# Kernel tuning notes

Hardware: AMD Instinct MI355X
Metric: run time of the kernel (lower is better)

Reference implementation:

```python
import jax, jax.numpy as jnp
import numpy as np
from jax import lax

B, L, D, H = 32, 512, 1024, 1024


def setup_inputs() -> dict:
    key = jax.random.key(0)
    kx, kw, kb = jax.random.split(key, 3)
    x = jax.random.normal(kx, (B, L, D), dtype=jnp.float32)
    # nn.Linear(D+H, 4H): weight (4H, D+H), bias (4H,), uniform(-1/sqrt(fan_in), 1/sqrt(fan_in))
    bound = 1.0 / np.sqrt(D + H)
    W = jax.random.uniform(kw, (4 * H, D + H), minval=-bound, maxval=bound, dtype=jnp.float32)
    b = jax.random.uniform(kb, (4 * H,), minval=-bound, maxval=bound, dtype=jnp.float32)
    return {"x": x, "W": W, "b": b}


def reference(x, W, b):
    Bsz, Lseq, Din = x.shape
    Hd = W.shape[0] // 4

    def step(carry, x_t):
        h, c = carry
        combined = jnp.concatenate([h, x_t], axis=-1)          # (B, H+D)
        gates = combined @ W.T + b                              # (B, 4H)
        f, i, o, c_tilde = jnp.split(gates, 4, axis=-1)
        c_new = jax.nn.sigmoid(f) * c + jax.nn.sigmoid(i) * jnp.tanh(c_tilde)
        h_new = jax.nn.sigmoid(o) * jnp.tanh(c_new)
        return (h_new, c_new), h_new

    h0 = jnp.zeros((Bsz, Hd), dtype=x.dtype)
    c0 = jnp.zeros((Bsz, Hd), dtype=x.dtype)
    xs = jnp.transpose(x, (1, 0, 2))                            # (L, B, D)
    _, hs = lax.scan(step, (h0, c0), xs)                        # hs: (L, B, H)
    return jnp.transpose(hs, (1, 0, 2))                         # (B, L, H)
```

## Files before the change

kernel.cpp:

```cpp
#include <hip/hip_runtime.h>
#include <hip/hip_fp16.h>

#define B_SZ 32
#define L_SZ 512
#define D_SZ 1024
#define H_SZ 1024
#define NG   4096
#define M_SZ 16384

typedef __attribute__((ext_vector_type(8))) short short8;
typedef __attribute__((ext_vector_type(4))) float f32x4;
typedef __attribute__((ext_vector_type(4))) unsigned u32x4;
typedef __attribute__((ext_vector_type(4))) unsigned short u16x4;

static const size_t GX_OFF  = 0;
static const size_t XB_OFF  = 134217728;
static const size_t WH_OFF  = 167772160;
static const size_t WX_OFF  = 176160768;
static const size_t FLG_OFF = 184680448;

__device__ __forceinline__ unsigned short f2bf(float f) {
  union { float f; unsigned u; } v; v.f = f;
  unsigned r = v.u + 0x7fffu + ((v.u >> 16) & 1u);
  return (unsigned short)(r >> 16);
}

__device__ __forceinline__ void gload_lds16(const void* g, void* l) {
  __builtin_amdgcn_global_load_lds(
      (const __attribute__((address_space(1))) unsigned*)g,
      (__attribute__((address_space(3))) unsigned*)l, 16, 0, 0);
}


__global__ __launch_bounds__(256) void k_convert_w(const float* __restrict__ W,
                                                   unsigned short* __restrict__ Wh,
                                                   unsigned short* __restrict__ Wx) {
  int idx = blockIdx.x * 256 + threadIdx.x;
  f32x4 v = ((const f32x4*)W)[idx];
  u16x4 o;
#pragma unroll
  for (int e = 0; e < 4; ++e) o[e] = f2bf(v[e]);
  int n   = idx >> 9;
  int col = (idx & 511) * 4;
  if (col < 1024) *(u16x4*)(Wh + (size_t)n * 1024 + col)          = o;
  else            *(u16x4*)(Wx + (size_t)n * 1024 + (col - 1024)) = o;
}

__global__ __launch_bounds__(256) void k_convert_x(const float* __restrict__ x,
                                                   unsigned short* __restrict__ xb) {
  int idx = blockIdx.x * 256 + threadIdx.x;
  f32x4 v = ((const f32x4*)x)[idx];
  u16x4 o;
#pragma unroll
  for (int e = 0; e < 4; ++e) o[e] = f2bf(v[e]);
  unsigned long long val;
  __builtin_memcpy(&val, &o, 8);
  unsigned short* p = xb + (size_t)idx * 4;
  asm volatile("global_store_dwordx2 %0, %1, off sc0 sc1"
               :: "v"(p), "v"(val) : "memory");
}

__global__ __launch_bounds__(256) void k_zero_wt(unsigned* __restrict__ p, int n) {
  int i = blockIdx.x * 256 + threadIdx.x;
  unsigned z = 0u;
  if (i < n)
    asm volatile("global_store_dword %0, %1, off sc0 sc1"
                 :: "v"(p + i), "v"(z) : "memory");
}


__global__ __launch_bounds__(256) void k_xgemm(const unsigned short* __restrict__ A,
                                               const unsigned short* __restrict__ Bw,
                                               __half* __restrict__ C) {
  __shared__ unsigned short sA[128 * 64];
  __shared__ unsigned short sB[128 * 64];
  const int m0 = blockIdx.x * 128;
  const int n0 = blockIdx.y * 128;
  const int tid = threadIdx.x;
  const int lane = tid & 63;
  const int w = tid >> 6;
  const int wm = w >> 1, wn = w & 1;
  f32x4 acc[4][4] = {};
  for (int k0 = 0; k0 < 1024; k0 += 64) {
#pragma unroll
    for (int it = 0; it < 4; ++it) {
      int chunk = it * 256 + w * 64 + lane;
      int row = chunk >> 3, kc = chunk & 7;
      gload_lds16(A + (size_t)(m0 + row) * 1024 + k0 + kc * 8,
                  (char*)sA + (size_t)(it * 256 + w * 64) * 16);
      gload_lds16(Bw + (size_t)(n0 + row) * 1024 + k0 + kc * 8,
                  (char*)sB + (size_t)(it * 256 + w * 64) * 16);
    }
    asm volatile("s_waitcnt vmcnt(0)" ::: "memory");
    __syncthreads();
#pragma unroll
    for (int ks = 0; ks < 2; ++ks) {
      short8 af[4], bfr[4];
#pragma unroll
      for (int i = 0; i < 4; ++i) {
        int arow = wm * 64 + i * 16 + (lane & 15);
        af[i] = *(const short8*)(sA + arow * 64 + ks * 32 + (lane >> 4) * 8);
      }
#pragma unroll
      for (int j = 0; j < 4; ++j) {
        int brow = wn * 64 + j * 16 + (lane & 15);
        bfr[j] = *(const short8*)(sB + brow * 64 + ks * 32 + (lane >> 4) * 8);
      }
#pragma unroll
      for (int i = 0; i < 4; ++i)
#pragma unroll
        for (int j = 0; j < 4; ++j)
          acc[i][j] = __builtin_amdgcn_mfma_f32_16x16x32_bf16(af[i], bfr[j], acc[i][j], 0, 0, 0);
    }
    __syncthreads();
  }
#pragma unroll
  for (int i = 0; i < 4; ++i)
#pragma unroll
    for (int j = 0; j < 4; ++j)
#pragma unroll
      for (int q = 0; q < 4; ++q) {
        int row = m0 + wm * 64 + i * 16 + (lane >> 4) * 4 + q;
        int col = n0 + wn * 64 + j * 16 + (lane & 15);
        C[(size_t)row * NG + col] = __float2half(acc[i][j][q]);
      }
}


__global__ __launch_bounds__(256) void k_lstm(const unsigned short* __restrict__ Whg,
                                              const __half* __restrict__ Gx,
                                              const float* __restrict__ bias,
                                              unsigned short* __restrict__ ring,
                                              float* __restrict__ out,
                                              unsigned* __restrict__ flags) {
  extern __shared__ char lds[];
  char* w_base = lds;
  char* h_base = lds + 65536;
  float* gates_s = (float*)(lds + 131072);
  float* bias_s  = (float*)(lds + 131072 + 4224);
  float* c_s     = (float*)(lds + 131072 + 4224 + 128);
  unsigned short* hlds = (unsigned short*)(lds + 131072 + 4224 + 128 + 1024);

  const int tid = threadIdx.x;
  const int lane = tid & 63;
  const int w = tid >> 6;
  const int wg = blockIdx.x;
  const int j0 = wg * 8;

  __builtin_amdgcn_fence(__ATOMIC_ACQUIRE, "agent");

  for (int i = tid; i < 4096; i += 256) {
    int c = i >> 7, kc = i & 127;
    int n = (c >> 3) * 1024 + j0 + (c & 7);
    u32x4 v = *(const u32x4*)(Whg + (size_t)n * 1024 + kc * 8);
    *(u32x4*)(w_base + c * 2048 + ((kc * 16) ^ ((c & 7) << 4))) = v;
  }
  if (tid < 32) bias_s[tid] = bias[(tid >> 3) * 1024 + j0 + (tid & 7)];
  c_s[tid] = 0.f;
  __syncthreads();

  const int mt = w >> 1, nt = w & 1;
  const int arow = mt * 16 + (lane & 15);
  const int brow = nt * 16 + (lane & 15);
  const char* aBase = h_base + arow * 2048;
  const char* bBase = w_base + brow * 2048;
  const int kslot = (lane >> 4) * 16;
  const int aswz = (arow & 7) << 4;
  const int bswz = (brow & 7) << 4;
  const int b_ = tid >> 3, jj = tid & 7;
  const float rb0 = bias_s[jj], rb1 = bias_s[8 + jj];
  const float rb2 = bias_s[16 + jj], rb3 = bias_s[24 + jj];

  const unsigned* fp0 = flags + (size_t)(2 * tid) * 16;
  const unsigned* fp1 = flags + (size_t)(2 * tid + 1) * 16;

  for (int t = 0; t < 512; ++t) {
    const unsigned short* hin = ring + (size_t)t * 32768;
    unsigned short* hout = (unsigned short*)ring + (size_t)(t + 1) * 32768;

    u32x4 hz = {0u, 0u, 0u, 0u};
    u32x4 h0=hz,h1=hz,h2=hz,h3=hz,h4=hz,h5=hz,h6=hz,h7=hz,
          h8=hz,h9=hz,h10=hz,h11=hz,h12=hz,h13=hz,h14=hz,h15=hz;
    if (t) {
#define HLD(r, it) asm volatile("global_load_dwordx4 %0, %1, off" \
      : "=v"(r) : "v"((const char*)hin + (size_t)((it) * 256 + tid) * 16) : "memory")
      HLD(h0,0); HLD(h1,1); HLD(h2,2); HLD(h3,3);
      HLD(h4,4); HLD(h5,5); HLD(h6,6); HLD(h7,7);
      HLD(h8,8); HLD(h9,9); HLD(h10,10); HLD(h11,11);
      HLD(h12,12); HLD(h13,13); HLD(h14,14); HLD(h15,15);
#undef HLD
    }
    const char* gxp = (const char*)(Gx + ((size_t)(b_ * L_SZ + t)) * NG + j0 + jj);
    unsigned gxa, gxb, gxc, gxd;
    asm volatile("global_load_ushort %0, %1, off" : "=v"(gxa) : "v"(gxp)        : "memory");
    asm volatile("global_load_ushort %0, %1, off" : "=v"(gxb) : "v"(gxp + 2048) : "memory");
    asm volatile("global_load_ushort %0, %1, off" : "=v"(gxc) : "v"(gxp + 4096) : "memory");
    asm volatile("global_load_ushort %0, %1, off" : "=v"(gxd) : "v"(gxp + 6144) : "memory");

#define HWR(r, it) { int i_ = (it) * 256 + tid; int bb_ = i_ >> 7, kc_ = i_ & 127; \
      *(u32x4*)(h_base + bb_ * 2048 + ((kc_ * 16) ^ ((bb_ & 7) << 4))) = r; }
    asm volatile("s_waitcnt vmcnt(12)" ::: "memory");
    HWR(h0,0); HWR(h1,1); HWR(h2,2); HWR(h3,3);
    HWR(h4,4); HWR(h5,5); HWR(h6,6); HWR(h7,7);
    asm volatile("s_waitcnt vmcnt(4)" ::: "memory");
    HWR(h8,8); HWR(h9,9); HWR(h10,10); HWR(h11,11);
    HWR(h12,12); HWR(h13,13); HWR(h14,14); HWR(h15,15);
#undef HWR
    __syncthreads();

    f32x4 acc = {0.f, 0.f, 0.f, 0.f};
#pragma unroll
    for (int ks = 0; ks < 32; ++ks) {
      int kb = ks * 64 + kslot;
      short8 a  = *(const short8*)(aBase + (kb ^ aswz));
      short8 bv = *(const short8*)(bBase + (kb ^ bswz));
      acc = __builtin_amdgcn_mfma_f32_16x16x32_bf16(a, bv, acc, 0, 0, 0);
    }
    __syncthreads();
#pragma unroll
    for (int q = 0; q < 4; ++q)
      gates_s[(mt * 16 + (lane >> 4) * 4 + q) * 33 + nt * 16 + (lane & 15)] = acc[q];
    __syncthreads();

    asm volatile("s_waitcnt vmcnt(0)" ::: "memory");
    float hn;
    {
      float sf = gates_s[b_ * 33 + jj]      + __half2float(__ushort_as_half((unsigned short)gxa)) + rb0;
      float si = gates_s[b_ * 33 + 8 + jj]  + __half2float(__ushort_as_half((unsigned short)gxb)) + rb1;
      float so = gates_s[b_ * 33 + 16 + jj] + __half2float(__ushort_as_half((unsigned short)gxc)) + rb2;
      float sc = gates_s[b_ * 33 + 24 + jj] + __half2float(__ushort_as_half((unsigned short)gxd)) + rb3;
      float gf = 1.f / (1.f + expf(-sf));
      float gi = 1.f / (1.f + expf(-si));
      float go = 1.f / (1.f + expf(-so));
      float cn = gf * c_s[tid] + gi * tanhf(sc);
      hn = go * tanhf(cn);
      c_s[tid] = cn;
      hlds[b_ * 8 + jj] = f2bf(hn);
    }
    float* outp = out + ((size_t)b_ * L_SZ + t) * H_SZ + j0 + jj;

    if (t < 511) {
      __syncthreads();
      if (tid < 32) {
        u32x4 v = *(u32x4*)(hlds + tid * 8);
        unsigned short* hp = hout + (size_t)tid * H_SZ + j0;
        asm volatile("global_store_dwordx4 %0, %1, off sc0 sc1"
                     :: "v"(hp), "v"(v) : "memory");
      }
      asm volatile("s_waitcnt vmcnt(0)" ::: "memory");
      if (tid == 0) {
        unsigned fv = (unsigned)(t + 1);
        const unsigned* myf = flags + (size_t)wg * 16;
        asm volatile("global_store_dword %0, %1, off sc0 sc1"
                     :: "v"(myf), "v"(fv) : "memory");
      }
      *outp = hn;
      if (tid < 64) {
        unsigned fa, fb;
        do {
          asm volatile("global_load_dword %0, %2, off sc0 sc1\n\t"
                       "global_load_dword %1, %3, off sc0 sc1\n\t"
                       "s_waitcnt vmcnt(0)"
                       : "=v"(fa), "=v"(fb) : "v"(fp0), "v"(fp1) : "memory");
        } while (!__all(fa > (unsigned)t && fb > (unsigned)t));
      }
      __syncthreads();
    } else {
      *outp = hn;
    }
  }
}


extern "C" void kernel_launch(void* const* d_in, const int* in_sizes, int n_in,
                              void* d_out, int out_size, void* d_ws, size_t ws_size,
                              hipStream_t stream) {
  const float* x = (const float*)d_in[0];
  const float* W = (const float*)d_in[1];
  const float* b = (const float*)d_in[2];
  char* ws = (char*)d_ws;
  __half* Gx           = (__half*)(ws + GX_OFF);
  unsigned short* xb   = (unsigned short*)(ws + XB_OFF);
  unsigned short* Wh   = (unsigned short*)(ws + WH_OFF);
  unsigned short* Wx   = (unsigned short*)(ws + WX_OFF);
  unsigned* flags      = (unsigned*)(ws + FLG_OFF);
  float* out = (float*)d_out;

  k_convert_w<<<8192, 256, 0, stream>>>(W, Wh, Wx);
  k_convert_x<<<16384, 256, 0, stream>>>(x, xb);
  k_zero_wt<<<8, 256, 0, stream>>>(flags, 8192 / 4);

  k_xgemm<<<dim3(128, 32), 256, 0, stream>>>(xb, Wx, Gx);

  hipFuncSetAttribute((const void*)k_lstm,
                      hipFuncAttributeMaxDynamicSharedMemorySize, 137472);
  k_lstm<<<128, 256, 137472, stream>>>(Wh, Gx, b, xb, out, flags);
}
```

Before: 2.389 ms.

## Load recurrent h MFMA fragments directly from global into registers, skip LDS staging

The recurrent step no longer stages the previous hidden state through LDS. Each lane loads its own MFMA A-operand fragments straight from the global ring buffer into registers, and staged vmcnt waits overlap those loads with MFMAs split across two accumulators. This removes the LDS write, a barrier and the LDS reads from the serial per-step critical path, and it shrinks LDS use. The cell state also moves from LDS into a register. The cost is higher VGPR pressure from 32 vector registers of h per lane, and each wave refetches h rows redundantly from global/L2.

```diff
diff --git a/kernel.cpp b/kernel.cpp
--- a/kernel.cpp
+++ b/kernel.cpp
@@ -127,19 +127,17 @@
 }
 
 
-__global__ __launch_bounds__(256) void k_lstm(const unsigned short* __restrict__ Whg,
-                                              const __half* __restrict__ Gx,
-                                              const float* __restrict__ bias,
-                                              unsigned short* __restrict__ ring,
-                                              float* __restrict__ out,
-                                              unsigned* __restrict__ flags) {
+__global__ __launch_bounds__(256, 1) void k_lstm(const unsigned short* __restrict__ Whg,
+                                                 const __half* __restrict__ Gx,
+                                                 const float* __restrict__ bias,
+                                                 unsigned short* __restrict__ ring,
+                                                 float* __restrict__ out,
+                                                 unsigned* __restrict__ flags) {
   extern __shared__ char lds[];
   char* w_base = lds;
-  char* h_base = lds + 65536;
-  float* gates_s = (float*)(lds + 131072);
-  float* bias_s  = (float*)(lds + 131072 + 4224);
-  float* c_s     = (float*)(lds + 131072 + 4224 + 128);
-  unsigned short* hlds = (unsigned short*)(lds + 131072 + 4224 + 128 + 1024);
+  float* gates_s = (float*)(lds + 65536);
+  float* bias_s  = (float*)(lds + 65536 + 4224);
+  unsigned short* hlds = (unsigned short*)(lds + 65536 + 4224 + 128);
 
   const int tid = threadIdx.x;
   const int lane = tid & 63;
@@ -156,40 +154,26 @@
     *(u32x4*)(w_base + c * 2048 + ((kc * 16) ^ ((c & 7) << 4))) = v;
   }
   if (tid < 32) bias_s[tid] = bias[(tid >> 3) * 1024 + j0 + (tid & 7)];
-  c_s[tid] = 0.f;
   __syncthreads();
 
   const int mt = w >> 1, nt = w & 1;
-  const int arow = mt * 16 + (lane & 15);
   const int brow = nt * 16 + (lane & 15);
-  const char* aBase = h_base + arow * 2048;
   const char* bBase = w_base + brow * 2048;
   const int kslot = (lane >> 4) * 16;
-  const int aswz = (arow & 7) << 4;
   const int bswz = (brow & 7) << 4;
   const int b_ = tid >> 3, jj = tid & 7;
   const float rb0 = bias_s[jj], rb1 = bias_s[8 + jj];
   const float rb2 = bias_s[16 + jj], rb3 = bias_s[24 + jj];
+  const size_t a_off = (size_t)(mt * 16 + (lane & 15)) * 2048 + (size_t)(lane >> 4) * 16;
+  float c_reg = 0.f;
 
   const unsigned* fp0 = flags + (size_t)(2 * tid) * 16;
   const unsigned* fp1 = flags + (size_t)(2 * tid + 1) * 16;
 
   for (int t = 0; t < 512; ++t) {
-    const unsigned short* hin = ring + (size_t)t * 32768;
-    unsigned short* hout = (unsigned short*)ring + (size_t)(t + 1) * 32768;
-
-    u32x4 hz = {0u, 0u, 0u, 0u};
-    u32x4 h0=hz,h1=hz,h2=hz,h3=hz,h4=hz,h5=hz,h6=hz,h7=hz,
-          h8=hz,h9=hz,h10=hz,h11=hz,h12=hz,h13=hz,h14=hz,h15=hz;
-    if (t) {
-#define HLD(r, it) asm volatile("global_load_dwordx4 %0, %1, off" \
-      : "=v"(r) : "v"((const char*)hin + (size_t)((it) * 256 + tid) * 16) : "memory")
-      HLD(h0,0); HLD(h1,1); HLD(h2,2); HLD(h3,3);
-      HLD(h4,4); HLD(h5,5); HLD(h6,6); HLD(h7,7);
-      HLD(h8,8); HLD(h9,9); HLD(h10,10); HLD(h11,11);
-      HLD(h12,12); HLD(h13,13); HLD(h14,14); HLD(h15,15);
-#undef HLD
-    }
+    const char* aG = (const char*)ring + (size_t)t * 65536 + a_off;
+    unsigned short* hout = ring + (size_t)(t + 1) * 32768;
+
     const char* gxp = (const char*)(Gx + ((size_t)(b_ * L_SZ + t)) * NG + j0 + jj);
     unsigned gxa, gxb, gxc, gxd;
     asm volatile("global_load_ushort %0, %1, off" : "=v"(gxa) : "v"(gxp)        : "memory");
@@ -197,26 +181,44 @@
     asm volatile("global_load_ushort %0, %1, off" : "=v"(gxc) : "v"(gxp + 4096) : "memory");
     asm volatile("global_load_ushort %0, %1, off" : "=v"(gxd) : "v"(gxp + 6144) : "memory");
 
-#define HWR(r, it) { int i_ = (it) * 256 + tid; int bb_ = i_ >> 7, kc_ = i_ & 127; \
-      *(u32x4*)(h_base + bb_ * 2048 + ((kc_ * 16) ^ ((bb_ & 7) << 4))) = r; }
-    asm volatile("s_waitcnt vmcnt(12)" ::: "memory");
-    HWR(h0,0); HWR(h1,1); HWR(h2,2); HWR(h3,3);
-    HWR(h4,4); HWR(h5,5); HWR(h6,6); HWR(h7,7);
-    asm volatile("s_waitcnt vmcnt(4)" ::: "memory");
-    HWR(h8,8); HWR(h9,9); HWR(h10,10); HWR(h11,11);
-    HWR(h12,12); HWR(h13,13); HWR(h14,14); HWR(h15,15);
-#undef HWR
-    __syncthreads();
-
-    f32x4 acc = {0.f, 0.f, 0.f, 0.f};
-#pragma unroll
-    for (int ks = 0; ks < 32; ++ks) {
-      int kb = ks * 64 + kslot;
-      short8 a  = *(const short8*)(aBase + (kb ^ aswz));
-      short8 bv = *(const short8*)(bBase + (kb ^ bswz));
-      acc = __builtin_amdgcn_mfma_f32_16x16x32_bf16(a, bv, acc, 0, 0, 0);
-    }
-    __syncthreads();
+    u32x4 areg[32];
+    if (t) {
+#pragma unroll
+      for (int ks = 0; ks < 32; ++ks)
+        asm volatile("global_load_dwordx4 %0, %1, off offset:%2"
+                     : "=v"(areg[ks]) : "v"(aG), "n"(ks * 64) : "memory");
+    } else {
+#pragma unroll
+      for (int ks = 0; ks < 32; ++ks) areg[ks] = (u32x4){0u, 0u, 0u, 0u};
+    }
+
+    f32x4 acc0 = {0.f, 0.f, 0.f, 0.f}, acc1 = {0.f, 0.f, 0.f, 0.f};
+#pragma unroll
+    for (int g = 0; g < 4; ++g) {
+      short8 bfr[8];
+#pragma unroll
+      for (int k = 0; k < 8; ++k) {
+        int ks = g * 8 + k;
+        bfr[k] = *(const short8*)(bBase + ((ks * 64 + kslot) ^ bswz));
+      }
+      if (t) {
+        if (g == 0)      asm volatile("s_waitcnt vmcnt(24)" ::: "memory");
+        else if (g == 1) asm volatile("s_waitcnt vmcnt(16)" ::: "memory");
+        else if (g == 2) asm volatile("s_waitcnt vmcnt(8)"  ::: "memory");
+        else             asm volatile("s_waitcnt vmcnt(0)"  ::: "memory");
+        __builtin_amdgcn_sched_barrier(0);
+      }
+#pragma unroll
+      for (int k = 0; k < 8; k += 2) {
+        int ks = g * 8 + k;
+        short8 a0, a1;
+        __builtin_memcpy(&a0, &areg[ks], 16);
+        __builtin_memcpy(&a1, &areg[ks + 1], 16);
+        acc0 = __builtin_amdgcn_mfma_f32_16x16x32_bf16(a0, bfr[k],     acc0, 0, 0, 0);
+        acc1 = __builtin_amdgcn_mfma_f32_16x16x32_bf16(a1, bfr[k + 1], acc1, 0, 0, 0);
+      }
+    }
+    f32x4 acc = acc0 + acc1;
 #pragma unroll
     for (int q = 0; q < 4; ++q)
       gates_s[(mt * 16 + (lane >> 4) * 4 + q) * 33 + nt * 16 + (lane & 15)] = acc[q];
@@ -232,10 +234,10 @@
       float gf = 1.f / (1.f + expf(-sf));
       float gi = 1.f / (1.f + expf(-si));
       float go = 1.f / (1.f + expf(-so));
-      float cn = gf * c_s[tid] + gi * tanhf(sc);
+      float cn = gf * c_reg + gi * tanhf(sc);
       hn = go * tanhf(cn);
-      c_s[tid] = cn;
-      hlds[b_ * 8 + jj] = f2bf(hn);
+      c_reg = cn;
+      hlds[tid] = f2bf(hn);
     }
     float* outp = out + ((size_t)b_ * L_SZ + t) * H_SZ + j0 + jj;
 
@@ -293,6 +295,6 @@
   k_xgemm<<<dim3(128, 32), 256, 0, stream>>>(xb, Wx, Gx);
 
   hipFuncSetAttribute((const void*)k_lstm,
-                      hipFuncAttributeMaxDynamicSharedMemorySize, 137472);
-  k_lstm<<<128, 256, 137472, stream>>>(Wh, Gx, b, xb, out, flags);
-}
+                      hipFuncAttributeMaxDynamicSharedMemorySize, 70400);
+  k_lstm<<<128, 256, 70400, stream>>>(Wh, Gx, b, xb, out, flags);
+}
```

Result: slower. 3.546 ms (+48.4%).

## Keep recurrent weight slice in registers and split K across waves

Applied to the files above, without the earlier changes.

The recurrent LSTM kernel no longer stages its slice of Wh in LDS. Each wave holds its 256-wide K slice of the weight fragments in registers and computes all 32x32 gate outputs for that K range with four MFMA accumulators. The four per-wave partial sums are reduced through LDS, and the cell state moves from LDS to a register. This cuts LDS weight reads and the per-step LDS footprint, at the cost of higher register pressure (launch_bounds 256,1) and an extra partial-sum reduction on each step.

```diff
diff --git a/kernel.cpp b/kernel.cpp
--- a/kernel.cpp
+++ b/kernel.cpp
@@ -127,63 +127,65 @@
 }
 
 
-__global__ __launch_bounds__(256) void k_lstm(const unsigned short* __restrict__ Whg,
-                                              const __half* __restrict__ Gx,
-                                              const float* __restrict__ bias,
-                                              unsigned short* __restrict__ ring,
-                                              float* __restrict__ out,
-                                              unsigned* __restrict__ flags) {
+__global__ __launch_bounds__(256, 1) void k_lstm(const unsigned short* __restrict__ Whg,
+                                                 const __half* __restrict__ Gx,
+                                                 const float* __restrict__ bias,
+                                                 unsigned short* __restrict__ ring,
+                                                 float* __restrict__ out,
+                                                 unsigned* __restrict__ flags) {
   extern __shared__ char lds[];
-  char* w_base = lds;
-  char* h_base = lds + 65536;
-  float* gates_s = (float*)(lds + 131072);
-  float* bias_s  = (float*)(lds + 131072 + 4224);
-  float* c_s     = (float*)(lds + 131072 + 4224 + 128);
-  unsigned short* hlds = (unsigned short*)(lds + 131072 + 4224 + 128 + 1024);
+  char* h_base  = lds;
+  float* part   = (float*)(lds + 65536);
+  float* bias_s = (float*)(lds + 65536 + 18432);
+  unsigned short* hlds = (unsigned short*)(lds + 65536 + 18432 + 128);
 
   const int tid = threadIdx.x;
   const int lane = tid & 63;
-  const int w = tid >> 6;
+  const int wv = tid >> 6;
   const int wg = blockIdx.x;
   const int j0 = wg * 8;
 
   __builtin_amdgcn_fence(__ATOMIC_ACQUIRE, "agent");
 
-  for (int i = tid; i < 4096; i += 256) {
-    int c = i >> 7, kc = i & 127;
-    int n = (c >> 3) * 1024 + j0 + (c & 7);
-    u32x4 v = *(const u32x4*)(Whg + (size_t)n * 1024 + kc * 8);
-    *(u32x4*)(w_base + c * 2048 + ((kc * 16) ^ ((c & 7) << 4))) = v;
+  short8 bfrag[2][8];
+#pragma unroll
+  for (int ntx = 0; ntx < 2; ++ntx) {
+#pragma unroll
+    for (int ks = 0; ks < 8; ++ks) {
+      int br = ntx * 16 + (lane & 15);
+      const unsigned short* src = Whg
+          + (size_t)((br >> 3) * 1024 + j0 + (br & 7)) * 1024
+          + wv * 256 + ks * 32 + (lane >> 4) * 8;
+      bfrag[ntx][ks] = *(const short8*)src;
+    }
   }
   if (tid < 32) bias_s[tid] = bias[(tid >> 3) * 1024 + j0 + (tid & 7)];
-  c_s[tid] = 0.f;
   __syncthreads();
 
-  const int mt = w >> 1, nt = w & 1;
-  const int arow = mt * 16 + (lane & 15);
-  const int brow = nt * 16 + (lane & 15);
-  const char* aBase = h_base + arow * 2048;
-  const char* bBase = w_base + brow * 2048;
+  const int row0 = lane & 15;
+  const char* aB0 = h_base + row0 * 2048;
+  const char* aB1 = h_base + (16 + row0) * 2048;
   const int kslot = (lane >> 4) * 16;
-  const int aswz = (arow & 7) << 4;
-  const int bswz = (brow & 7) << 4;
+  const int aswz = (row0 & 7) << 4;
+  const int kbyte0 = wv * 512;
   const int b_ = tid >> 3, jj = tid & 7;
   const float rb0 = bias_s[jj], rb1 = bias_s[8 + jj];
   const float rb2 = bias_s[16 + jj], rb3 = bias_s[24 + jj];
+  float c_reg = 0.f;
 
   const unsigned* fp0 = flags + (size_t)(2 * tid) * 16;
   const unsigned* fp1 = flags + (size_t)(2 * tid + 1) * 16;
 
   for (int t = 0; t < 512; ++t) {
-    const unsigned short* hin = ring + (size_t)t * 32768;
-    unsigned short* hout = (unsigned short*)ring + (size_t)(t + 1) * 32768;
+    const char* hin = (const char*)ring + (size_t)t * 65536;
+    unsigned short* hout = ring + (size_t)(t + 1) * 32768;
 
     u32x4 hz = {0u, 0u, 0u, 0u};
     u32x4 h0=hz,h1=hz,h2=hz,h3=hz,h4=hz,h5=hz,h6=hz,h7=hz,
           h8=hz,h9=hz,h10=hz,h11=hz,h12=hz,h13=hz,h14=hz,h15=hz;
     if (t) {
 #define HLD(r, it) asm volatile("global_load_dwordx4 %0, %1, off" \
-      : "=v"(r) : "v"((const char*)hin + (size_t)((it) * 256 + tid) * 16) : "memory")
+      : "=v"(r) : "v"(hin + (size_t)((it) * 256 + tid) * 16) : "memory")
       HLD(h0,0); HLD(h1,1); HLD(h2,2); HLD(h3,3);
       HLD(h4,4); HLD(h5,5); HLD(h6,6); HLD(h7,7);
       HLD(h8,8); HLD(h9,9); HLD(h10,10); HLD(h11,11);
@@ -200,42 +202,62 @@
 #define HWR(r, it) { int i_ = (it) * 256 + tid; int bb_ = i_ >> 7, kc_ = i_ & 127; \
       *(u32x4*)(h_base + bb_ * 2048 + ((kc_ * 16) ^ ((bb_ & 7) << 4))) = r; }
     asm volatile("s_waitcnt vmcnt(12)" ::: "memory");
+    __builtin_amdgcn_sched_barrier(0);
     HWR(h0,0); HWR(h1,1); HWR(h2,2); HWR(h3,3);
     HWR(h4,4); HWR(h5,5); HWR(h6,6); HWR(h7,7);
     asm volatile("s_waitcnt vmcnt(4)" ::: "memory");
+    __builtin_amdgcn_sched_barrier(0);
     HWR(h8,8); HWR(h9,9); HWR(h10,10); HWR(h11,11);
     HWR(h12,12); HWR(h13,13); HWR(h14,14); HWR(h15,15);
 #undef HWR
     __syncthreads();
 
-    f32x4 acc = {0.f, 0.f, 0.f, 0.f};
-#pragma unroll
-    for (int ks = 0; ks < 32; ++ks) {
-      int kb = ks * 64 + kslot;
-      short8 a  = *(const short8*)(aBase + (kb ^ aswz));
-      short8 bv = *(const short8*)(bBase + (kb ^ bswz));
-      acc = __builtin_amdgcn_mfma_f32_16x16x32_bf16(a, bv, acc, 0, 0, 0);
+    f32x4 acc00 = {0.f,0.f,0.f,0.f}, acc01 = {0.f,0.f,0.f,0.f};
+    f32x4 acc10 = {0.f,0.f,0.f,0.f}, acc11 = {0.f,0.f,0.f,0.f};
+#pragma unroll
+    for (int ks = 0; ks < 8; ++ks) {
+      int kb = kbyte0 + ks * 64 + kslot;
+      short8 a0 = *(const short8*)(aB0 + (kb ^ aswz));
+      short8 a1 = *(const short8*)(aB1 + (kb ^ aswz));
+      acc00 = __builtin_amdgcn_mfma_f32_16x16x32_bf16(a0, bfrag[0][ks], acc00, 0, 0, 0);
+      acc01 = __builtin_amdgcn_mfma_f32_16x16x32_bf16(a0, bfrag[1][ks], acc01, 0, 0, 0);
+      acc10 = __builtin_amdgcn_mfma_f32_16x16x32_bf16(a1, bfrag[0][ks], acc10, 0, 0, 0);
+      acc11 = __builtin_amdgcn_mfma_f32_16x16x32_bf16(a1, bfrag[1][ks], acc11, 0, 0, 0);
+    }
+    {
+      float* pw = part + wv * 1152;
+      int r0 = (lane >> 4) * 4, cA = lane & 15;
+#pragma unroll
+      for (int q = 0; q < 4; ++q) {
+        pw[(r0 + q) * 36 + cA]           = acc00[q];
+        pw[(r0 + q) * 36 + 16 + cA]      = acc01[q];
+        pw[(16 + r0 + q) * 36 + cA]      = acc10[q];
+        pw[(16 + r0 + q) * 36 + 16 + cA] = acc11[q];
+      }
     }
     __syncthreads();
-#pragma unroll
-    for (int q = 0; q < 4; ++q)
-      gates_s[(mt * 16 + (lane >> 4) * 4 + q) * 33 + nt * 16 + (lane & 15)] = acc[q];
-    __syncthreads();
-
+
+    float s0 = 0.f, s1 = 0.f, s2 = 0.f, s3 = 0.f;
+#pragma unroll
+    for (int p = 0; p < 4; ++p) {
+      const float* pp = part + p * 1152 + b_ * 36 + jj;
+      s0 += pp[0]; s1 += pp[8]; s2 += pp[16]; s3 += pp[24];
+    }
     asm volatile("s_waitcnt vmcnt(0)" ::: "memory");
+    __builtin_amdgcn_sched_barrier(0);
     float hn;
     {
-      float sf = gates_s[b_ * 33 + jj]      + __half2float(__ushort_as_half((unsigned short)gxa)) + rb0;
-      float si = gates_s[b_ * 33 + 8 + jj]  + __half2float(__ushort_as_half((unsigned short)gxb)) + rb1;
-      float so = gates_s[b_ * 33 + 16 + jj] + __half2float(__ushort_as_half((unsigned short)gxc)) + rb2;
-      float sc = gates_s[b_ * 33 + 24 + jj] + __half2float(__ushort_as_half((unsigned short)gxd)) + rb3;
+      float sf = s0 + __half2float(__ushort_as_half((unsigned short)gxa)) + rb0;
+      float si = s1 + __half2float(__ushort_as_half((unsigned short)gxb)) + rb1;
+      float so = s2 + __half2float(__ushort_as_half((unsigned short)gxc)) + rb2;
+      float sc = s3 + __half2float(__ushort_as_half((unsigned short)gxd)) + rb3;
       float gf = 1.f / (1.f + expf(-sf));
       float gi = 1.f / (1.f + expf(-si));
       float go = 1.f / (1.f + expf(-so));
-      float cn = gf * c_s[tid] + gi * tanhf(sc);
+      float cn = gf * c_reg + gi * tanhf(sc);
       hn = go * tanhf(cn);
-      c_s[tid] = cn;
-      hlds[b_ * 8 + jj] = f2bf(hn);
+      c_reg = cn;
+      hlds[tid] = f2bf(hn);
     }
     float* outp = out + ((size_t)b_ * L_SZ + t) * H_SZ + j0 + jj;
 
@@ -292,7 +314,7 @@
 
   k_xgemm<<<dim3(128, 32), 256, 0, stream>>>(xb, Wx, Gx);
 
-  hipFuncSetAttribute((const void*)k_lstm,
-                      hipFuncAttributeMaxDynamicSharedMemorySize, 137472);
-  k_lstm<<<128, 256, 137472, stream>>>(Wh, Gx, b, xb, out, flags);
-}
+  (void)hipFuncSetAttribute((const void*)k_lstm,
+                            hipFuncAttributeMaxDynamicSharedMemorySize, 84608);
+  k_lstm<<<128, 256, 84608, stream>>>(Wh, Gx, b, xb, out, flags);
+}
```

Measured after the change: 2.163 ms. -9.4%, faster.
